# Optimization experiments

Measured on AMD Instinct MI355X. Metric: run time of the kernel, lower is better.

## Reference

```python
import jax, jax.numpy as jnp
import numpy as np

N_NODES = 100000
N_EDGES = 3200000
IN_CH, HID, OUT_CH = 128, 16, 64


def setup_inputs() -> dict:
    key = jax.random.key(0)
    k1, k2, k3, k4 = jax.random.split(key, 4)
    x = jax.random.normal(k1, (N_NODES, IN_CH), dtype=jnp.float32)
    edge_index = jax.random.randint(k2, (2, N_EDGES), 0, N_NODES, dtype=jnp.int32)
    # GCNConv params: lin weight (no bias) + separate bias added after aggregation
    W1 = jax.random.normal(k3, (IN_CH, HID), dtype=jnp.float32) * (1.0 / np.sqrt(IN_CH))
    b1 = jnp.zeros((HID,), dtype=jnp.float32)
    W2 = jax.random.normal(k4, (HID, OUT_CH), dtype=jnp.float32) * (1.0 / np.sqrt(HID))
    b2 = jnp.zeros((OUT_CH,), dtype=jnp.float32)
    return {"x": x, "edge_index": edge_index, "W1": W1, "b1": b1, "W2": W2, "b2": b2}


def _gcn_norm(edge_index, num_nodes):
    # PyG gcn_norm: add self-loops, symmetric deg^{-1/2} A_hat deg^{-1/2}
    loop = jnp.arange(num_nodes, dtype=edge_index.dtype)
    src = jnp.concatenate([edge_index[0], loop])
    dst = jnp.concatenate([edge_index[1], loop])
    ones = jnp.ones(src.shape[0], dtype=jnp.float32)
    deg = jax.ops.segment_sum(ones, dst, num_segments=num_nodes)
    dinv = jnp.where(deg > 0, jax.lax.rsqrt(deg), 0.0)
    norm = dinv[src] * dinv[dst]  # [E + N]
    return src, dst, norm


def _gcn_conv(x, src, dst, norm, W, b, num_nodes):
    h = x @ W                      # [N, out] transform first (cheap dims)
    msg = h[src] * norm[:, None]   # edge-indexed gather, [E+N, out]
    out = jax.ops.segment_sum(msg, dst, num_segments=num_nodes)  # scatter-add
    return out + b


def reference(x, edge_index, W1, b1, W2, b2):
    n = x.shape[0]
    src, dst, norm = _gcn_norm(edge_index, n)
    h = jax.nn.relu(_gcn_conv(x, src, dst, norm, W1, b1, n))
    return _gcn_conv(h, src, dst, norm, W2, b2, n)
```

## Files before the change

kernel.cpp:

```cpp
#include <hip/hip_runtime.h>
#include <hip/hip_bf16.h>

#define N_NODES 100000
#define N_EDGES 3200000
#define IN_CH 128
#define HID 16
#define OUT_CH 64
#define BSHIFT 9
#define BNODES 512
#define NBUCK 196
#define BCAP 18000
#define TR 32
#define XP 132
#define EPB 2048

__device__ __forceinline__ unsigned short f2bf(float f) {
    union { float f; unsigned v; } t; t.f = f;
    unsigned r = t.v + 0x7FFFu + ((t.v >> 16) & 1u);
    return (unsigned short)(r >> 16);
}
__device__ __forceinline__ unsigned pack2(float lo, float hi) {
    return (unsigned)f2bf(lo) | ((unsigned)f2bf(hi) << 16);
}
__device__ __forceinline__ void acc8(uint4 v, float* a) {
    union { unsigned u; float f; } c;
    c.u = v.x << 16;         a[0] += c.f;
    c.u = v.x & 0xffff0000u; a[1] += c.f;
    c.u = v.y << 16;         a[2] += c.f;
    c.u = v.y & 0xffff0000u; a[3] += c.f;
    c.u = v.z << 16;         a[4] += c.f;
    c.u = v.z & 0xffff0000u; a[5] += c.f;
    c.u = v.w << 16;         a[6] += c.f;
    c.u = v.w & 0xffff0000u; a[7] += c.f;
}

__global__ void k_init_cur(int* __restrict__ cur) {
    int t = threadIdx.x;
    if (t < NBUCK) cur[t] = t * BCAP;
}

__global__ __launch_bounds__(256) void k_bucket(const int* __restrict__ src, const int* __restrict__ dst,
                                                int* __restrict__ cur, unsigned* __restrict__ colp, int e) {
    __shared__ int lh[NBUCK];
    __shared__ int lb[NBUCK];
    int t = threadIdx.x;
    if (t < NBUCK) lh[t] = 0;
    __syncthreads();
    int base = blockIdx.x * EPB + t * 8;
    int bk[8]; int rk[8]; unsigned pk[8];
    if (base + 7 < e) {
        const int4* d4 = reinterpret_cast<const int4*>(dst + base);
        const int4* s4 = reinterpret_cast<const int4*>(src + base);
        int4 d0 = d4[0], d1 = d4[1];
        int4 s0 = s4[0], s1 = s4[1];
        int dd[8] = {d0.x, d0.y, d0.z, d0.w, d1.x, d1.y, d1.z, d1.w};
        int ss[8] = {s0.x, s0.y, s0.z, s0.w, s1.x, s1.y, s1.z, s1.w};
#pragma unroll
        for (int j = 0; j < 8; ++j) {
            int d = dd[j];
            bk[j] = d >> BSHIFT;
            pk[j] = ((unsigned)(d & (BNODES - 1)) << 17) | (unsigned)ss[j];
            rk[j] = atomicAdd(&lh[bk[j]], 1);
        }
    } else {
#pragma unroll
        for (int j = 0; j < 8; ++j) {
            int idx = base + j;
            if (idx < e) {
                int d = dst[idx];
                bk[j] = d >> BSHIFT;
                pk[j] = ((unsigned)(d & (BNODES - 1)) << 17) | (unsigned)src[idx];
                rk[j] = atomicAdd(&lh[bk[j]], 1);
            } else bk[j] = -1;
        }
    }
    __syncthreads();
    if (t < NBUCK) { int c = lh[t]; lb[t] = c ? atomicAdd(&cur[t], c) : 0; }
    __syncthreads();
#pragma unroll
    for (int j = 0; j < 8; ++j) if (bk[j] >= 0) colp[lb[bk[j]] + rk[j]] = pk[j];
}

__global__ __launch_bounds__(1024) void k_build(const unsigned* __restrict__ colp, const int* __restrict__ cur,
                                                int* __restrict__ col, int* __restrict__ row_ptr,
                                                int* __restrict__ deg, float* __restrict__ dinv) {
    __shared__ int cnt[BNODES];
    __shared__ int sc[BNODES];
    __shared__ int ex[BNODES];
    __shared__ int curl[BNODES];
    int b = blockIdx.x, t = threadIdx.x;
    if (t < BNODES) cnt[t] = 0;
    __syncthreads();
    int base = b * BCAP;
    int m = cur[b] - base;
    int i = t;
    for (; i + 3072 < m; i += 4096) {
        unsigned p0 = colp[base + i];
        unsigned p1 = colp[base + i + 1024];
        unsigned p2 = colp[base + i + 2048];
        unsigned p3 = colp[base + i + 3072];
        atomicAdd(&cnt[p0 >> 17], 1);
        atomicAdd(&cnt[p1 >> 17], 1);
        atomicAdd(&cnt[p2 >> 17], 1);
        atomicAdd(&cnt[p3 >> 17], 1);
    }
    for (; i < m; i += 1024) atomicAdd(&cnt[colp[base + i] >> 17], 1);
    __syncthreads();
    int v = 0;
    if (t < BNODES) { v = cnt[t]; sc[t] = v; }
    __syncthreads();
    for (int off = 1; off < BNODES; off <<= 1) {
        int x = 0;
        if (t < BNODES && t >= off) x = sc[t - off];
        __syncthreads();
        if (t < BNODES) sc[t] += x;
        __syncthreads();
    }
    if (t < BNODES) {
        ex[t] = sc[t] - v;
        curl[t] = 0;
        int node = b * BNODES + t;
        if (node < N_NODES) {
            row_ptr[node] = base + ex[t];
            deg[node] = v;
            dinv[node] = rsqrtf((float)v + 1.0f);
        }
    }
    __syncthreads();
    i = t;
    for (; i + 3072 < m; i += 4096) {
        unsigned p0 = colp[base + i];
        unsigned p1 = colp[base + i + 1024];
        unsigned p2 = colp[base + i + 2048];
        unsigned p3 = colp[base + i + 3072];
        int l0 = p0 >> 17, l1 = p1 >> 17, l2 = p2 >> 17, l3 = p3 >> 17;
        int q0 = atomicAdd(&curl[l0], 1);
        int q1 = atomicAdd(&curl[l1], 1);
        int q2 = atomicAdd(&curl[l2], 1);
        int q3 = atomicAdd(&curl[l3], 1);
        col[base + ex[l0] + q0] = (int)(p0 & 0x1FFFF);
        col[base + ex[l1] + q1] = (int)(p1 & 0x1FFFF);
        col[base + ex[l2] + q2] = (int)(p2 & 0x1FFFF);
        col[base + ex[l3] + q3] = (int)(p3 & 0x1FFFF);
    }
    for (; i < m; i += 1024) {
        unsigned pv = colp[base + i];
        int l = pv >> 17;
        int p = atomicAdd(&curl[l], 1);
        col[base + ex[l] + p] = (int)(pv & 0x1FFFF);
    }
}

__global__ __launch_bounds__(256) void k_gemm1(const float* __restrict__ x,
                                               const float* __restrict__ W1,
                                               const float* __restrict__ dinv,
                                               unsigned short* __restrict__ h1p, int n) {
    __shared__ float Wt[HID * XP];
    __shared__ float xs[TR * XP];
    int t = threadIdx.x;
    for (int i = t; i < HID * IN_CH; i += 256) {
        int k = i & 127, c = i >> 7;
        Wt[c * XP + k] = W1[k * HID + c];
    }
    int row0 = blockIdx.x * TR;
    for (int i = t; i < TR * IN_CH / 4; i += 256) {
        int r = i >> 5, c4 = i & 31;
        int row = row0 + r;
        float4 v = (row < n) ? reinterpret_cast<const float4*>(x)[(size_t)row * 32 + c4]
                             : make_float4(0.f, 0.f, 0.f, 0.f);
        *reinterpret_cast<float4*>(&xs[r * XP + c4 * 4]) = v;
    }
    __syncthreads();
    int r = t >> 4;
    int c = t & 15;
    const float4* xr0 = reinterpret_cast<const float4*>(&xs[r * XP]);
    const float4* xr1 = reinterpret_cast<const float4*>(&xs[(r + 16) * XP]);
    const float4* wc  = reinterpret_cast<const float4*>(&Wt[c * XP]);
    float a0 = 0.f, a1 = 0.f;
#pragma unroll 4
    for (int k4 = 0; k4 < IN_CH / 4; ++k4) {
        float4 wv  = wc[k4];
        float4 v0  = xr0[k4];
        float4 v1  = xr1[k4];
        a0 = fmaf(v0.x, wv.x, a0); a0 = fmaf(v0.y, wv.y, a0);
        a0 = fmaf(v0.z, wv.z, a0); a0 = fmaf(v0.w, wv.w, a0);
        a1 = fmaf(v1.x, wv.x, a1); a1 = fmaf(v1.y, wv.y, a1);
        a1 = fmaf(v1.z, wv.z, a1); a1 = fmaf(v1.w, wv.w, a1);
    }
    int rr0 = row0 + r, rr1 = rr0 + 16;
    if (rr0 < n) h1p[(size_t)rr0 * HID + c] = f2bf(dinv[rr0] * a0);
    if (rr1 < n) h1p[(size_t)rr1 * HID + c] = f2bf(dinv[rr1] * a1);
}

__global__ __launch_bounds__(256) void k_gather1(const unsigned short* __restrict__ h1p,
                                                 const int* __restrict__ row_ptr,
                                                 const int* __restrict__ deg,
                                                 const float* __restrict__ dinv,
                                                 const int* __restrict__ col,
                                                 const float* __restrict__ b1,
                                                 unsigned short* __restrict__ h2p, int n) {
    int t = blockIdx.x * blockDim.x + threadIdx.x;
    int i = t >> 2;
    if (i >= n) return;
    int q = t & 1, p = (t >> 1) & 1;
    const uint4* hp = reinterpret_cast<const uint4*>(h1p);
    float a[8] = {0, 0, 0, 0, 0, 0, 0, 0};
    int j0 = row_ptr[i], j1 = j0 + deg[i];
    int j = j0 + p;
    for (; j + 6 < j1; j += 8) {
        int s0 = col[j], s1 = col[j + 2], s2 = col[j + 4], s3 = col[j + 6];
        uint4 v0 = hp[(size_t)s0 * 2 + q];
        uint4 v1 = hp[(size_t)s1 * 2 + q];
        uint4 v2 = hp[(size_t)s2 * 2 + q];
        uint4 v3 = hp[(size_t)s3 * 2 + q];
        acc8(v0, a); acc8(v1, a); acc8(v2, a); acc8(v3, a);
    }
    for (; j < j1; j += 2) acc8(hp[(size_t)col[j] * 2 + q], a);
#pragma unroll
    for (int k = 0; k < 8; ++k) a[k] += __shfl_xor(a[k], 2);
    if (p == 0) {
        acc8(hp[(size_t)i * 2 + q], a);
        float di = dinv[i];
        float4 bl = *reinterpret_cast<const float4*>(&b1[q * 8]);
        float4 bh = *reinterpret_cast<const float4*>(&b1[q * 8 + 4]);
        float o[8];
        o[0] = di * fmaxf(fmaf(di, a[0], bl.x), 0.f);
        o[1] = di * fmaxf(fmaf(di, a[1], bl.y), 0.f);
        o[2] = di * fmaxf(fmaf(di, a[2], bl.z), 0.f);
        o[3] = di * fmaxf(fmaf(di, a[3], bl.w), 0.f);
        o[4] = di * fmaxf(fmaf(di, a[4], bh.x), 0.f);
        o[5] = di * fmaxf(fmaf(di, a[5], bh.y), 0.f);
        o[6] = di * fmaxf(fmaf(di, a[6], bh.z), 0.f);
        o[7] = di * fmaxf(fmaf(di, a[7], bh.w), 0.f);
        uint4 ov;
        ov.x = pack2(o[0], o[1]);
        ov.y = pack2(o[2], o[3]);
        ov.z = pack2(o[4], o[5]);
        ov.w = pack2(o[6], o[7]);
        reinterpret_cast<uint4*>(h2p)[(size_t)i * 2 + q] = ov;
    }
}

__global__ __launch_bounds__(256) void k_gather2_out(const unsigned short* __restrict__ h2p,
                                                     const int* __restrict__ row_ptr,
                                                     const int* __restrict__ deg,
                                                     const float* __restrict__ dinv,
                                                     const int* __restrict__ col,
                                                     const float* __restrict__ W2,
                                                     const float* __restrict__ b2,
                                                     float* __restrict__ out, int n) {
    __shared__ float Ws[HID * OUT_CH];
    __shared__ float as[64][HID + 1];
    int t = threadIdx.x;
    for (int i = t; i < HID * OUT_CH; i += 256) Ws[i] = W2[i];
    int nl = t >> 2;
    int i = blockIdx.x * 64 + nl;
    int q = t & 1, p = (t >> 1) & 1;
    const uint4* hp = reinterpret_cast<const uint4*>(h2p);
    if (i < n) {
        float a[8] = {0, 0, 0, 0, 0, 0, 0, 0};
        int j0 = row_ptr[i], j1 = j0 + deg[i];
        int j = j0 + p;
        for (; j + 6 < j1; j += 8) {
            int s0 = col[j], s1 = col[j + 2], s2 = col[j + 4], s3 = col[j + 6];
            uint4 v0 = hp[(size_t)s0 * 2 + q];
            uint4 v1 = hp[(size_t)s1 * 2 + q];
            uint4 v2 = hp[(size_t)s2 * 2 + q];
            uint4 v3 = hp[(size_t)s3 * 2 + q];
            acc8(v0, a); acc8(v1, a); acc8(v2, a); acc8(v3, a);
        }
        for (; j < j1; j += 2) acc8(hp[(size_t)col[j] * 2 + q], a);
#pragma unroll
        for (int k = 0; k < 8; ++k) a[k] += __shfl_xor(a[k], 2);
        if (p == 0) {
            acc8(hp[(size_t)i * 2 + q], a);
            float di = dinv[i];
#pragma unroll
            for (int k = 0; k < 8; ++k) as[nl][q * 8 + k] = di * a[k];
        }
    } else if (p == 0) {
#pragma unroll
        for (int k = 0; k < 8; ++k) as[nl][q * 8 + k] = 0.f;
    }
    __syncthreads();
    int g = t & 3;
    float r[16];
#pragma unroll
    for (int c = 0; c < 16; ++c) r[c] = b2[g * 16 + c];
#pragma unroll
    for (int k = 0; k < HID; ++k) {
        float a = as[nl][k];
#pragma unroll
        for (int c = 0; c < 16; ++c) r[c] = fmaf(a, Ws[k * OUT_CH + g * 16 + c], r[c]);
    }
    if (i < n) {
        float* op = &out[(size_t)i * OUT_CH + g * 16];
#pragma unroll
        for (int c = 0; c < 16; c += 4)
            *reinterpret_cast<float4*>(&op[c]) = make_float4(r[c], r[c + 1], r[c + 2], r[c + 3]);
    }
}

extern "C" void kernel_launch(void* const* d_in, const int* in_sizes, int n_in,
                              void* d_out, int out_size, void* d_ws, size_t ws_size,
                              hipStream_t stream) {
    const float* x  = (const float*)d_in[0];
    const int*   ei = (const int*)d_in[1];
    const float* W1 = (const float*)d_in[2];
    const float* b1 = (const float*)d_in[3];
    const float* W2 = (const float*)d_in[4];
    const float* b2 = (const float*)d_in[5];
    float* out = (float*)d_out;

    const int* src = ei;
    const int* dst = ei + N_EDGES;

    int*            cur     = (int*)d_ws;
    int*            row_ptr = cur + 256;
    int*            deg     = row_ptr + N_NODES;
    float*          dinv    = (float*)(deg + N_NODES);
    int*            col     = (int*)(dinv + N_NODES);
    unsigned short* h1p     = (unsigned short*)(col + NBUCK * BCAP);
    unsigned*       colp    = (unsigned*)((int*)h1p + 800000);
    unsigned short* h2p     = (unsigned short*)colp;

    k_init_cur<<<1, 256, 0, stream>>>(cur);
    k_bucket<<<(N_EDGES + EPB - 1) / EPB, 256, 0, stream>>>(src, dst, cur, colp, N_EDGES);
    k_build<<<NBUCK, 1024, 0, stream>>>(colp, cur, col, row_ptr, deg, dinv);

    k_gemm1<<<(N_NODES + TR - 1) / TR, 256, 0, stream>>>(x, W1, dinv, h1p, N_NODES);

    k_gather1<<<((size_t)4 * N_NODES + 255) / 256, 256, 0, stream>>>(h1p, row_ptr, deg, dinv, col,
                                                                     b1, h2p, N_NODES);

    k_gather2_out<<<(N_NODES + 63) / 64, 256, 0, stream>>>(h2p, row_ptr, deg, dinv, col, W2, b2,
                                                           out, N_NODES);
}
```

Baseline: 158.3 us.

## Replicate bucket cursors and stage edges in shared memory for coalesced scatter

Bucket cursors are split into 8 replicas per bucket, chosen by block index, to reduce global atomic contention. Each block now handles 4096 edges, sorts them by bucket in LDS through a prefix scan, and writes them out contiguously so the colp stores coalesce. k_build walks the 8 replica segments, two at a time in the counting pass. Per-replica capacity is 2304, which relies on the uniform-random edge distribution and could overflow on skewed inputs.

```diff
diff --git a/kernel.cpp b/kernel.cpp
--- a/kernel.cpp
+++ b/kernel.cpp
@@ -9,10 +9,12 @@
 #define BSHIFT 9
 #define BNODES 512
 #define NBUCK 196
-#define BCAP 18000
+#define NREP 8
+#define BCAPR 2304
+#define BCAPB (NREP * BCAPR)
 #define TR 32
 #define XP 132
-#define EPB 2048
+#define EPB 4096
 
 __device__ __forceinline__ unsigned short f2bf(float f) {
     union { float f; unsigned v; } t; t.f = f;
@@ -35,36 +37,39 @@
 }
 
 __global__ void k_init_cur(int* __restrict__ cur) {
-    int t = threadIdx.x;
-    if (t < NBUCK) cur[t] = t * BCAP;
+    int i = blockIdx.x * blockDim.x + threadIdx.x;
+    if (i < NBUCK * NREP) cur[i] = i * BCAPR;
 }
 
 __global__ __launch_bounds__(256) void k_bucket(const int* __restrict__ src, const int* __restrict__ dst,
                                                 int* __restrict__ cur, unsigned* __restrict__ colp, int e) {
     __shared__ int lh[NBUCK];
+    __shared__ int lbase[NBUCK];
     __shared__ int lb[NBUCK];
+    __shared__ int sh[256];
+    __shared__ unsigned ebuf[EPB];
+    __shared__ unsigned char ebkt[EPB];
     int t = threadIdx.x;
     if (t < NBUCK) lh[t] = 0;
     __syncthreads();
-    int base = blockIdx.x * EPB + t * 8;
-    int bk[8]; int rk[8]; unsigned pk[8];
-    if (base + 7 < e) {
+    int base = blockIdx.x * EPB + t * 16;
+    int bk[16]; int rk[16]; unsigned pk[16];
+    if (base + 15 < e) {
+        union { int4 v4[4]; int v[16]; } D, S;
         const int4* d4 = reinterpret_cast<const int4*>(dst + base);
         const int4* s4 = reinterpret_cast<const int4*>(src + base);
-        int4 d0 = d4[0], d1 = d4[1];
-        int4 s0 = s4[0], s1 = s4[1];
-        int dd[8] = {d0.x, d0.y, d0.z, d0.w, d1.x, d1.y, d1.z, d1.w};
-        int ss[8] = {s0.x, s0.y, s0.z, s0.w, s1.x, s1.y, s1.z, s1.w};
-#pragma unroll
-        for (int j = 0; j < 8; ++j) {
-            int d = dd[j];
+        D.v4[0] = d4[0]; D.v4[1] = d4[1]; D.v4[2] = d4[2]; D.v4[3] = d4[3];
+        S.v4[0] = s4[0]; S.v4[1] = s4[1]; S.v4[2] = s4[2]; S.v4[3] = s4[3];
+#pragma unroll
+        for (int j = 0; j < 16; ++j) {
+            int d = D.v[j];
             bk[j] = d >> BSHIFT;
-            pk[j] = ((unsigned)(d & (BNODES - 1)) << 17) | (unsigned)ss[j];
+            pk[j] = ((unsigned)(d & (BNODES - 1)) << 17) | (unsigned)S.v[j];
             rk[j] = atomicAdd(&lh[bk[j]], 1);
         }
     } else {
 #pragma unroll
-        for (int j = 0; j < 8; ++j) {
+        for (int j = 0; j < 16; ++j) {
             int idx = base + j;
             if (idx < e) {
                 int d = dst[idx];
@@ -75,10 +80,32 @@
         }
     }
     __syncthreads();
-    if (t < NBUCK) { int c = lh[t]; lb[t] = c ? atomicAdd(&cur[t], c) : 0; }
-    __syncthreads();
-#pragma unroll
-    for (int j = 0; j < 8; ++j) if (bk[j] >= 0) colp[lb[bk[j]] + rk[j]] = pk[j];
+    int v = (t < NBUCK) ? lh[t] : 0;
+    sh[t] = v;
+    __syncthreads();
+    for (int off = 1; off < 256; off <<= 1) {
+        int x = (t >= off) ? sh[t - off] : 0;
+        __syncthreads();
+        sh[t] += x;
+        __syncthreads();
+    }
+    if (t < NBUCK) lbase[t] = sh[t] - v;
+    int rep = blockIdx.x & (NREP - 1);
+    if (t < NBUCK) lb[t] = v ? atomicAdd(&cur[t * NREP + rep], v) : 0;
+#pragma unroll
+    for (int j = 0; j < 16; ++j) {
+        if (bk[j] >= 0) {
+            int pos = lbase[bk[j]] + rk[j];
+            ebuf[pos] = pk[j];
+            ebkt[pos] = (unsigned char)bk[j];
+        }
+    }
+    __syncthreads();
+    int tot = sh[255];
+    for (int i = t; i < tot; i += 256) {
+        int b = ebkt[i];
+        colp[lb[b] + (i - lbase[b])] = ebuf[i];
+    }
 }
 
 __global__ __launch_bounds__(1024) void k_build(const unsigned* __restrict__ colp, const int* __restrict__ cur,
@@ -91,20 +118,25 @@
     int b = blockIdx.x, t = threadIdx.x;
     if (t < BNODES) cnt[t] = 0;
     __syncthreads();
-    int base = b * BCAP;
-    int m = cur[b] - base;
-    int i = t;
-    for (; i + 3072 < m; i += 4096) {
-        unsigned p0 = colp[base + i];
-        unsigned p1 = colp[base + i + 1024];
-        unsigned p2 = colp[base + i + 2048];
-        unsigned p3 = colp[base + i + 3072];
-        atomicAdd(&cnt[p0 >> 17], 1);
-        atomicAdd(&cnt[p1 >> 17], 1);
-        atomicAdd(&cnt[p2 >> 17], 1);
-        atomicAdd(&cnt[p3 >> 17], 1);
-    }
-    for (; i < m; i += 1024) atomicAdd(&cnt[colp[base + i] >> 17], 1);
+    int rb[NREP], mr[NREP];
+#pragma unroll
+    for (int r = 0; r < NREP; ++r) {
+        rb[r] = (b * NREP + r) * BCAPR;
+        mr[r] = cur[b * NREP + r] - rb[r];
+    }
+#pragma unroll
+    for (int r = 0; r < NREP; r += 2) {
+        int i0 = t, i1 = t;
+        for (;;) {
+            bool a0 = i0 < mr[r], a1 = i1 < mr[r + 1];
+            if (!a0 && !a1) break;
+            unsigned p0 = a0 ? colp[rb[r] + i0] : 0;
+            unsigned p1 = a1 ? colp[rb[r + 1] + i1] : 0;
+            if (a0) atomicAdd(&cnt[p0 >> 17], 1);
+            if (a1) atomicAdd(&cnt[p1 >> 17], 1);
+            i0 += 1024; i1 += 1024;
+        }
+    }
     __syncthreads();
     int v = 0;
     if (t < BNODES) { v = cnt[t]; sc[t] = v; }
@@ -116,38 +148,26 @@
         if (t < BNODES) sc[t] += x;
         __syncthreads();
     }
+    int colbase = b * BCAPB;
     if (t < BNODES) {
         ex[t] = sc[t] - v;
         curl[t] = 0;
         int node = b * BNODES + t;
         if (node < N_NODES) {
-            row_ptr[node] = base + ex[t];
+            row_ptr[node] = colbase + ex[t];
             deg[node] = v;
             dinv[node] = rsqrtf((float)v + 1.0f);
         }
     }
     __syncthreads();
-    i = t;
-    for (; i + 3072 < m; i += 4096) {
-        unsigned p0 = colp[base + i];
-        unsigned p1 = colp[base + i + 1024];
-        unsigned p2 = colp[base + i + 2048];
-        unsigned p3 = colp[base + i + 3072];
-        int l0 = p0 >> 17, l1 = p1 >> 17, l2 = p2 >> 17, l3 = p3 >> 17;
-        int q0 = atomicAdd(&curl[l0], 1);
-        int q1 = atomicAdd(&curl[l1], 1);
-        int q2 = atomicAdd(&curl[l2], 1);
-        int q3 = atomicAdd(&curl[l3], 1);
-        col[base + ex[l0] + q0] = (int)(p0 & 0x1FFFF);
-        col[base + ex[l1] + q1] = (int)(p1 & 0x1FFFF);
-        col[base + ex[l2] + q2] = (int)(p2 & 0x1FFFF);
-        col[base + ex[l3] + q3] = (int)(p3 & 0x1FFFF);
-    }
-    for (; i < m; i += 1024) {
-        unsigned pv = colp[base + i];
-        int l = pv >> 17;
-        int p = atomicAdd(&curl[l], 1);
-        col[base + ex[l] + p] = (int)(pv & 0x1FFFF);
+#pragma unroll
+    for (int r = 0; r < NREP; ++r) {
+        for (int i = t; i < mr[r]; i += 1024) {
+            unsigned pv = colp[rb[r] + i];
+            int l = pv >> 17;
+            int p = atomicAdd(&curl[l], 1);
+            col[colbase + ex[l] + p] = (int)(pv & 0x1FFFF);
+        }
     }
 }
 
@@ -316,15 +336,15 @@
     const int* dst = ei + N_EDGES;
 
     int*            cur     = (int*)d_ws;
-    int*            row_ptr = cur + 256;
+    int*            row_ptr = cur + 1600;
     int*            deg     = row_ptr + N_NODES;
     float*          dinv    = (float*)(deg + N_NODES);
     int*            col     = (int*)(dinv + N_NODES);
-    unsigned short* h1p     = (unsigned short*)(col + NBUCK * BCAP);
+    unsigned short* h1p     = (unsigned short*)(col + NBUCK * BCAPB);
     unsigned*       colp    = (unsigned*)((int*)h1p + 800000);
     unsigned short* h2p     = (unsigned short*)colp;
 
-    k_init_cur<<<1, 256, 0, stream>>>(cur);
+    k_init_cur<<<(NBUCK * NREP + 255) / 256, 256, 0, stream>>>(cur);
     k_bucket<<<(N_EDGES + EPB - 1) / EPB, 256, 0, stream>>>(src, dst, cur, colp, N_EDGES);
     k_build<<<NBUCK, 1024, 0, stream>>>(colp, cur, col, row_ptr, deg, dinv);
 
```

Result: faster. 147.6 us (-6.8%).
